# Optimization experiments

Measured on AMD Instinct MI355X. Metric: run time of the kernel, lower is better.

## Reference

```python
import jax, jax.numpy as jnp
import numpy as np

B = 4
N_PER_B = 65536
N = B * N_PER_B
GROUP_SIZE = 64
ORDER = 9  # min bits to cover grid size 512
C0, C1, C2 = 64, 128, 128


def hilbert_encode(coors, order):
    """Skilling AxesToTranspose, vectorized over N points, 3 dims -> int32 code."""
    n = 3
    X = [coors[:, i].astype(jnp.int32) for i in range(n)]
    M = 1 << (order - 1)
    Q = M
    while Q > 1:
        P = Q - 1
        for i in range(n):
            cond = (X[i] & Q) != 0
            if i == 0:
                X[0] = jnp.where(cond, X[0] ^ P, X[0])
            else:
                t = (X[0] ^ X[i]) & P
                x0 = jnp.where(cond, X[0] ^ P, X[0] ^ t)
                xi = jnp.where(cond, X[i], X[i] ^ t)
                X[0], X[i] = x0, xi
        Q >>= 1
    for i in range(1, n):
        X[i] = X[i] ^ X[i - 1]
    t = jnp.zeros_like(X[0])
    Q = M
    while Q > 1:
        t = jnp.where((X[n - 1] & Q) != 0, t ^ (Q - 1), t)
        Q >>= 1
    X = [x ^ t for x in X]
    # interleave transposed bits MSB-first: code has 3*order bits (27 < 31, fits int32)
    code = jnp.zeros_like(X[0])
    for b in range(order - 1, -1, -1):
        for i in range(n):
            code = (code << 1) | ((X[i] >> b) & 1)
    return code


def _mapping_indices(vox_coors):
    """Two Hilbert orderings (normal + reversed coord axes); per-batch stable grouping."""
    batch = vox_coors[:, 0]
    c1 = vox_coors[:, 1:4]
    c2 = vox_coors[:, 3:0:-1]  # [0,3,2,1] reverse of the xyz columns
    code1 = hilbert_encode(c1, ORDER)
    code2 = hilbert_encode(c2, ORDER)
    ind1 = jnp.lexsort((code1, batch))  # batch-major, curve-order minor
    ind2 = jnp.lexsort((code2, batch))
    inv1 = jnp.argsort(ind1)
    ind12 = inv1[ind2]  # maps ordering-1 arrangement to ordering-2 arrangement
    return ind1, ind12


def _block(p, x, params):
    """VoxFormer-style block: center pts per group, pos-encode, gate feats, local attn, FFN."""
    Wpos, bpos, Wq, Wk, Wv, Wo, Wout = params
    C = Wq.shape[0]
    gs = GROUP_SIZE
    pg = p.reshape(-1, gs, 3)
    e = (pg - pg.mean(axis=1, keepdims=True)).reshape(-1, 3) @ Wpos + bpos  # [N,C]
    h = (x * e).reshape(-1, gs, C)  # [G,gs,C]
    q, k, v = h @ Wq, h @ Wk, h @ Wv
    scores = jnp.einsum('gqc,gkc->gqk', q, k) / jnp.sqrt(jnp.asarray(C, q.dtype))
    attn = jax.nn.softmax(scores, axis=-1)
    o = jnp.einsum('gqk,gkc->gqc', attn, v).reshape(-1, C) @ Wo
    return jax.nn.relu(o) @ Wout  # [N,C_out]


def setup_inputs() -> dict:
    key = jax.random.key(0)
    ks = jax.random.split(key, 20)
    bcol = jnp.repeat(jnp.arange(B, dtype=jnp.int32), N_PER_B)
    z = jax.random.randint(ks[0], (N,), 0, 64, dtype=jnp.int32)
    y = jax.random.randint(ks[1], (N,), 0, 512, dtype=jnp.int32)
    x = jax.random.randint(ks[2], (N,), 0, 512, dtype=jnp.int32)
    vox_coors = jnp.stack([bcol, z, y, x], axis=1)
    vox_numbs = jnp.full((B,), N_PER_B, dtype=jnp.int32)
    vox_feats = jax.random.normal(ks[3], (N, C0), dtype=jnp.float32)
    pts_coors = jax.random.normal(ks[4], (N, 3), dtype=jnp.float32)
    s = lambda k, shape: jax.random.normal(k, shape, dtype=jnp.float32) / np.float32(np.sqrt(shape[0]))
    return dict(
        vox_numbs=vox_numbs, vox_coors=vox_coors, vox_feats=vox_feats, pts_coors=pts_coors,
        Wpos1=s(ks[5], (3, C0)), bpos1=jnp.zeros((C0,), jnp.float32),
        Wq1=s(ks[6], (C0, C0)), Wk1=s(ks[7], (C0, C0)), Wv1=s(ks[8], (C0, C0)),
        Wo1=s(ks[9], (C0, C0)), Wout1=s(ks[10], (C0, C1)),
        Wpos2=s(ks[11], (3, C1)), bpos2=jnp.zeros((C1,), jnp.float32),
        Wq2=s(ks[12], (C1, C1)), Wk2=s(ks[13], (C1, C1)), Wv2=s(ks[14], (C1, C1)),
        Wo2=s(ks[15], (C1, C1)), Wout2=s(ks[16], (C1, C2)),
    )


def reference(vox_numbs, vox_coors, vox_feats, pts_coors,
              Wpos1, bpos1, Wq1, Wk1, Wv1, Wo1, Wout1,
              Wpos2, bpos2, Wq2, Wk2, Wv2, Wo2, Wout2):
    ind1, ind12 = _mapping_indices(vox_coors)
    params = ((Wpos1, bpos1, Wq1, Wk1, Wv1, Wo1, Wout1),
              (Wpos2, bpos2, Wq2, Wk2, Wv2, Wo2, Wout2))
    for ind, prm in zip((ind1, ind12), params):
        vox_feats = vox_feats[ind]
        pts_coors = pts_coors[ind]
        vox_coors = vox_coors[ind]
        vox_feats = _block(pts_coors, vox_feats, prm)
    return vox_feats, pts_coors, vox_coors, vox_numbs
```

## Files before the change

### kernel.cpp

```cpp
#include <hip/hip_runtime.h>

using u64 = unsigned long long;
typedef _Float16 f16;
using f16x8 = __attribute__((ext_vector_type(8))) _Float16;
using f16x4 = __attribute__((ext_vector_type(4))) _Float16;
using f32x4 = __attribute__((ext_vector_type(4))) float;

__device__ __forceinline__ int hilbert3(int X0, int X1, int X2) {
  #pragma unroll
  for (int Q = 256; Q > 1; Q >>= 1) {
    const int P = Q - 1;
    if (X0 & Q) X0 ^= P;
    int t1 = (X0 ^ X1) & P;
    if (X1 & Q) X0 ^= P; else { X0 ^= t1; X1 ^= t1; }
    int t2 = (X0 ^ X2) & P;
    if (X2 & Q) X0 ^= P; else { X0 ^= t2; X2 ^= t2; }
  }
  X1 ^= X0;
  X2 ^= X1;
  int t = 0;
  #pragma unroll
  for (int Q = 256; Q > 1; Q >>= 1) if (X2 & Q) t ^= (Q - 1);
  X0 ^= t; X1 ^= t; X2 ^= t;
  int code = 0;
  #pragma unroll
  for (int b = 8; b >= 0; b--)
    code = (code << 3) | (((X0 >> b) & 1) << 2) | (((X1 >> b) & 1) << 1) | ((X2 >> b) & 1);
  return code;
}

__device__ __forceinline__ void cswap(u64& a, u64& b, bool up) {
  if ((a > b) == up) { u64 t = a; a = b; b = t; }
}

__global__ __launch_bounds__(1024) void sort_tile0(const int* __restrict__ vox,
                                                   u64* __restrict__ keys, int n,
                                                   int spanm1) {
  __shared__ u64 s[4096];
  const int base = blockIdx.x * 4096;
  const int bl = base & spanm1;
  #pragma unroll
  for (int m = 0; m < 4; m++) {
    const int e = base + threadIdx.x + m * 1024;
    const int isrc = e & (n - 1);
    const int4 c = ((const int4*)vox)[isrc];
    const unsigned code = (e < n) ? (unsigned)hilbert3(c.y, c.z, c.w)
                                  : (unsigned)hilbert3(c.w, c.z, c.y);
    s[threadIdx.x + m * 1024] =
        ((u64)(unsigned)c.x << 45) | ((u64)code << 18) | (unsigned)isrc;
  }
  __syncthreads();
  for (int k = 2; k <= 4096; k <<= 1) {
    for (int j = k >> 1; j >= 1; j >>= 1) {
      #pragma unroll
      for (int m = 0; m < 2; m++) {
        const int p = threadIdx.x + m * 1024;
        const int i = ((p & ~(j - 1)) << 1) | (p & (j - 1));
        const bool up = (((bl + i) & k) == 0);
        u64 a = s[i], b = s[i | j];
        if ((a > b) == up) { s[i] = b; s[i | j] = a; }
      }
      __syncthreads();
    }
  }
  #pragma unroll
  for (int m = 0; m < 4; m++)
    keys[base + threadIdx.x + m * 1024] = s[threadIdx.x + m * 1024];
}

template<int LEV>
__device__ __forceinline__ void gstepT(u64* __restrict__ keys, int t, int jlow,
                                       int k, int spanm1) {
  constexpr int S = 1 << LEV;
  const int i0 = ((t & ~(jlow - 1)) << LEV) | (t & (jlow - 1));
  const bool up = (((i0 & spanm1) & k) == 0);
  u64 x[S];
  #pragma unroll
  for (int m = 0; m < S; m++) x[m] = keys[i0 + (size_t)m * jlow];
  #pragma unroll
  for (int d = S >> 1; d >= 1; d >>= 1)
    #pragma unroll
    for (int m = 0; m < S; m++)
      if (!(m & d)) cswap(x[m], x[m | d], up);
  #pragma unroll
  for (int m = 0; m < S; m++) keys[i0 + (size_t)m * jlow] = x[m];
}

__global__ void bitonic_gN(u64* __restrict__ keys, int jlow, int lev, int k, int spanm1) {
  const int t = blockIdx.x * blockDim.x + threadIdx.x;
  switch (lev) {
    case 1: gstepT<1>(keys, t, jlow, k, spanm1); break;
    case 2: gstepT<2>(keys, t, jlow, k, spanm1); break;
    case 3: gstepT<3>(keys, t, jlow, k, spanm1); break;
    default: gstepT<4>(keys, t, jlow, k, spanm1); break;
  }
}

__global__ __launch_bounds__(1024) void merge_tile4(u64* __restrict__ keys, int k,
                                                    int spanm1) {
  __shared__ u64 s[4096];
  const int base = blockIdx.x * 4096;
  #pragma unroll
  for (int m = 0; m < 4; m++)
    s[threadIdx.x + m * 1024] = keys[base + threadIdx.x + m * 1024];
  __syncthreads();
  const bool up = (((base & spanm1) & k) == 0);
  for (int j = 2048; j >= 1; j >>= 1) {
    #pragma unroll
    for (int m = 0; m < 2; m++) {
      const int p = threadIdx.x + m * 1024;
      const int i = ((p & ~(j - 1)) << 1) | (p & (j - 1));
      u64 a = s[i], b = s[i | j];
      if ((a > b) == up) { s[i] = b; s[i | j] = a; }
    }
    __syncthreads();
  }
  #pragma unroll
  for (int m = 0; m < 4; m++)
    keys[base + threadIdx.x + m * 1024] = s[threadIdx.x + m * 1024];
}

__global__ void extract_inv_k(const u64* __restrict__ keys, const float* __restrict__ pts,
                              int* __restrict__ ind, int* __restrict__ inv,
                              float* __restrict__ pts1p, int n) {
  int t = blockIdx.x * blockDim.x + threadIdx.x;
  if (t >= n) return;
  int s = (int)(keys[t] & 0x3FFFFULL);
  ind[t] = s;
  inv[s] = t;
  pts1p[t * 3 + 0] = pts[s * 3 + 0];
  pts1p[t * 3 + 1] = pts[s * 3 + 1];
  pts1p[t * 3 + 2] = pts[s * 3 + 2];
}

__global__ void finish_k(const u64* __restrict__ keys2, const int* __restrict__ inv1,
                         int* __restrict__ g2, const float* __restrict__ pts,
                         const int* __restrict__ vox, const int* __restrict__ numbs,
                         float* __restrict__ out_pts, float* __restrict__ out_vox,
                         float* __restrict__ out_nb, int n, int B) {
  int t = blockIdx.x * blockDim.x + threadIdx.x;
  if (t >= n) return;
  int s = (int)(keys2[t] & 0x3FFFFULL);
  g2[t] = inv1[s];
  out_pts[t * 3 + 0] = pts[s * 3 + 0];
  out_pts[t * 3 + 1] = pts[s * 3 + 1];
  out_pts[t * 3 + 2] = pts[s * 3 + 2];
  const int4 v = ((const int4*)vox)[s];
  out_vox[t * 4 + 0] = (float)v.x;
  out_vox[t * 4 + 1] = (float)v.y;
  out_vox[t * 4 + 2] = (float)v.z;
  out_vox[t * 4 + 3] = (float)v.w;
  if (t < B) out_nb[t] = (float)numbs[t];
}

__global__ void prep_all(const float* __restrict__ Wq1, const float* __restrict__ Wk1,
                         const float* __restrict__ Wv1, const float* __restrict__ Wo1,
                         const float* __restrict__ Wout1,
                         const float* __restrict__ Wq2, const float* __restrict__ Wk2,
                         const float* __restrict__ Wv2, const float* __restrict__ Wo2,
                         const float* __restrict__ Wout2,
                         f16* __restrict__ A1a, f16* __restrict__ A2a, f16* __restrict__ A3a,
                         f16* __restrict__ A1b, f16* __restrict__ A2b, f16* __restrict__ A3b) {
  const int idx = blockIdx.x * blockDim.x + threadIdx.x;
  if (idx < 4096) {
    const int a = idx >> 6, b = idx & 63;
    float s1 = 0.f, s2 = 0.f;
    for (int c = 0; c < 64; c++) {
      s1 = fmaf(Wq1[b * 64 + c], Wk1[a * 64 + c], s1);
      s2 = fmaf(Wv1[b * 64 + c], Wo1[c * 64 + a], s2);
    }
    A1a[idx] = (f16)(s1 * 0.125f);
    A2a[idx] = (f16)s2;
  }
  if (idx < 8192) {
    const int o = idx >> 6, c = idx & 63;
    A3a[idx] = (f16)Wout1[c * 128 + o];
  }
  {
    const int a = idx >> 7, b = idx & 127;
    float s1 = 0.f, s2 = 0.f;
    for (int c = 0; c < 128; c++) {
      s1 = fmaf(Wq2[b * 128 + c], Wk2[a * 128 + c], s1);
      s2 = fmaf(Wv2[b * 128 + c], Wo2[c * 128 + a], s2);
    }
    A1b[idx] = (f16)(s1 * 0.08838834764831845f);
    A2b[idx] = (f16)s2;
    A3b[idx] = (f16)Wout2[b * 128 + a];
  }
}

__device__ __forceinline__ int swzb(int row) {
  return (((row & 7) ^ (((row >> 3) & 3) << 1)) << 4);
}

template<int M, int K, int AMODE>
__device__ __forceinline__ void gemmT(const f16* __restrict__ lA,
                                      const f16* __restrict__ lB, int w, int lane,
                                      f32x4 (&acc)[M / 64][4]) {
  constexpr int CT = M / 64;
  const int lr = lane & 15, lk = lane >> 4;
  #pragma unroll
  for (int ks = 0; ks < K / 32; ks++) {
    const int k0 = ks * 32 + lk * 8;
    f16x8 Af[CT];
    #pragma unroll
    for (int ct = 0; ct < CT; ct++) {
      const int c = lr + (w * CT + ct) * 16;
      if (AMODE == 1) {
        Af[ct] = *(const f16x8*)((const char*)lA + (((c * K + k0) * 2) ^ swzb(c)));
      } else {
        f16x8 a;
        #pragma unroll
        for (int e = 0; e < 8; e++) {
          const int j = k0 + e;
          a[e] = *(const f16*)((const char*)lA + (((j * M + c) * 2) ^ swzb(j)));
        }
        Af[ct] = a;
      }
    }
    f16x8 Bf[4];
    #pragma unroll
    for (int qt = 0; qt < 4; qt++) {
      const int q = lr + qt * 16;
      Bf[qt] = *(const f16x8*)((const char*)lB + (((q * K + k0) * 2) ^ swzb(q)));
    }
    __builtin_amdgcn_s_setprio(1);
    #pragma unroll
    for (int ct = 0; ct < CT; ct++)
      #pragma unroll
      for (int qt = 0; qt < 4; qt++)
        acc[ct][qt] = __builtin_amdgcn_mfma_f32_16x16x32_f16(Af[ct], Bf[qt], acc[ct][qt], 0, 0, 0);
    __builtin_amdgcn_s_setprio(0);
  }
}

template<int M, int K>
__device__ __forceinline__ void gemmPre(const f16x8 (&Af)[K / 32][M / 64],
                                        const f16* __restrict__ lB, int lane,
                                        f32x4 (&acc)[M / 64][4]) {
  constexpr int CT = M / 64;
  const int lr = lane & 15, lk = lane >> 4;
  #pragma unroll
  for (int ks = 0; ks < K / 32; ks++) {
    const int k0 = ks * 32 + lk * 8;
    f16x8 Bf[4];
    #pragma unroll
    for (int qt = 0; qt < 4; qt++) {
      const int q = lr + qt * 16;
      Bf[qt] = *(const f16x8*)((const char*)lB + (((q * K + k0) * 2) ^ swzb(q)));
    }
    __builtin_amdgcn_s_setprio(1);
    #pragma unroll
    for (int ct = 0; ct < CT; ct++)
      #pragma unroll
      for (int qt = 0; qt < 4; qt++)
        acc[ct][qt] = __builtin_amdgcn_mfma_f32_16x16x32_f16(Af[ks][ct], Bf[qt], acc[ct][qt], 0, 0, 0);
    __builtin_amdgcn_s_setprio(0);
  }
}

template<int M, int K>
__device__ __forceinline__ void loadA(const f16* __restrict__ Ag, int w, int lane,
                                      f16x8 (&Af)[K / 32][M / 64]) {
  constexpr int CT = M / 64;
  const int lr = lane & 15, lk = lane >> 4;
  #pragma unroll
  for (int ks = 0; ks < K / 32; ks++)
    #pragma unroll
    for (int ct = 0; ct < CT; ct++)
      Af[ks][ct] = *(const f16x8*)(Ag + (size_t)(lr + (w * CT + ct) * 16) * K + ks * 32 + lk * 8);
}

template<int M, bool RELU>
__device__ __forceinline__ void storeT16(f16* __restrict__ dst, int w, int lane,
                                         const f32x4 (&acc)[M / 64][4]) {
  constexpr int CT = M / 64;
  #pragma unroll
  for (int ct = 0; ct < CT; ct++)
    #pragma unroll
    for (int qt = 0; qt < 4; qt++) {
      const int q = (lane & 15) + qt * 16;
      const int c0 = (w * CT + ct) * 16 + (lane >> 4) * 4;
      f16x4 v;
      #pragma unroll
      for (int r = 0; r < 4; r++) {
        float x = acc[ct][qt][r];
        if (RELU) x = fmaxf(x, 0.f);
        v[r] = (f16)x;
      }
      *(f16x4*)((char*)dst + (((q * M + c0) * 2) ^ swzb(q))) = v;
    }
}

template<int C, bool X16, bool OUT16>
__global__ __launch_bounds__(512, 4) void block_mfma(
    const int* __restrict__ idx_x, const float* __restrict__ ptsP,
    const void* __restrict__ xsrc,
    const float* __restrict__ Wpos, const float* __restrict__ bpos,
    const f16* __restrict__ A1, const f16* __restrict__ A2, const f16* __restrict__ A3,
    void* __restrict__ outp) {
  constexpr int CT = C / 64;
  constexpr int GSZ = 64 * C * 4 + 8192;
  extern __shared__ char smem_raw[];
  char* smem = smem_raw + (threadIdx.x >> 8) * GSZ;
  f16* bufH = (f16*)smem;
  f16* bufT = bufH + 64 * C;
  f16* scH  = bufT + 64 * C;

  const int g = blockIdx.x * 2 + (threadIdx.x >> 8);
  const int t = threadIdx.x & 255;
  const int lane = t & 63;
  const int w = t >> 6;

  f16x8 A1f[C / 32][CT], A2f[C / 32][CT];
  loadA<C, C>(A1, w, lane, A1f);
  loadA<C, C>(A2, w, lane, A2f);

  const int q = t >> 2, qq = t & 3;
  const int sx = idx_x[g * 64 + q];
  f16x8 xr16[C / 32];
  float xv32[X16 ? 1 : C / 4];
  if (X16) {
    #pragma unroll
    for (int i = 0; i < C / 32; i++)
      xr16[i] = *(const f16x8*)((const f16*)xsrc + (size_t)sx * C + qq * (C / 4) + i * 8);
  } else {
    #pragma unroll
    for (int i = 0; i < C / 16; i++) {
      float4 x0 = *(const float4*)((const float*)xsrc + (size_t)sx * C + qq * (C / 4) + i * 4);
      xv32[i * 4 + 0] = x0.x; xv32[i * 4 + 1] = x0.y;
      xv32[i * 4 + 2] = x0.z; xv32[i * 4 + 3] = x0.w;
    }
  }

  {
    float mx = ptsP[(g * 64 + lane) * 3 + 0];
    float my = ptsP[(g * 64 + lane) * 3 + 1];
    float mz = ptsP[(g * 64 + lane) * 3 + 2];
    #pragma unroll
    for (int o = 32; o > 0; o >>= 1) {
      mx += __shfl_xor(mx, o); my += __shfl_xor(my, o); mz += __shfl_xor(mz, o);
    }
    mx *= (1.f / 64.f); my *= (1.f / 64.f); mz *= (1.f / 64.f);

    const float d0 = ptsP[(g * 64 + q) * 3 + 0] - mx;
    const float d1 = ptsP[(g * 64 + q) * 3 + 1] - my;
    const float d2 = ptsP[(g * 64 + q) * 3 + 2] - mz;
    #pragma unroll
    for (int i = 0; i < C / 32; i++) {
      const int c0 = qq * (C / 4) + i * 8;
      f16x8 hv;
      #pragma unroll
      for (int jj = 0; jj < 8; jj += 4) {
        const float4 w0 = *(const float4*)(Wpos + 0 * C + c0 + jj);
        const float4 w1 = *(const float4*)(Wpos + 1 * C + c0 + jj);
        const float4 w2 = *(const float4*)(Wpos + 2 * C + c0 + jj);
        const float4 bb = *(const float4*)(bpos + c0 + jj);
        float xa = X16 ? (float)xr16[i][jj + 0] : xv32[i * 8 + jj + 0];
        float xb = X16 ? (float)xr16[i][jj + 1] : xv32[i * 8 + jj + 1];
        float xc = X16 ? (float)xr16[i][jj + 2] : xv32[i * 8 + jj + 2];
        float xd = X16 ? (float)xr16[i][jj + 3] : xv32[i * 8 + jj + 3];
        hv[jj + 0] = (f16)(xa * fmaf(d0, w0.x, fmaf(d1, w1.x, fmaf(d2, w2.x, bb.x))));
        hv[jj + 1] = (f16)(xb * fmaf(d0, w0.y, fmaf(d1, w1.y, fmaf(d2, w2.y, bb.y))));
        hv[jj + 2] = (f16)(xc * fmaf(d0, w0.z, fmaf(d1, w1.z, fmaf(d2, w2.z, bb.z))));
        hv[jj + 3] = (f16)(xd * fmaf(d0, w0.w, fmaf(d1, w1.w, fmaf(d2, w2.w, bb.w))));
      }
      *(f16x8*)((char*)bufH + (((q * C + c0) * 2) ^ swzb(q))) = hv;
    }
  }
  __syncthreads();

  {
    f32x4 acc[CT][4] = {};
    gemmPre<C, C>(A1f, bufH, lane, acc);
    storeT16<C, false>(bufT, w, lane, acc);
  }
  __syncthreads();

  {
    f32x4 acc[1][4] = {};
    gemmT<64, C, 1>(bufH, bufT, w, lane, acc);
    const int lr = lane & 15, lk = lane >> 4;
    #pragma unroll
    for (int qt = 0; qt < 4; qt++) {
      const int qr = lr + qt * 16;
      const int j0 = w * 16 + lk * 4;
      f16x4 v;
      #pragma unroll
      for (int r = 0; r < 4; r++) v[r] = (f16)acc[0][qt][r];
      *(f16x4*)((char*)scH + (((qr * 64 + j0) * 2) ^ swzb(qr))) = v;
    }
  }
  __syncthreads();

  {
    float v[16];
    float mxv = -3.0e38f;
    #pragma unroll
    for (int i = 0; i < 2; i++) {
      f16x8 x8 = *(const f16x8*)((const char*)scH + (((q * 64 + qq * 16 + i * 8) * 2) ^ swzb(q)));
      #pragma unroll
      for (int j = 0; j < 8; j++) {
        v[i * 8 + j] = (float)x8[j];
        mxv = fmaxf(mxv, v[i * 8 + j]);
      }
    }
    mxv = fmaxf(mxv, __shfl_xor(mxv, 1));
    mxv = fmaxf(mxv, __shfl_xor(mxv, 2));
    float s = 0.f;
    #pragma unroll
    for (int i = 0; i < 16; i++) { v[i] = __expf(v[i] - mxv); s += v[i]; }
    s += __shfl_xor(s, 1);
    s += __shfl_xor(s, 2);
    const float inv = 1.f / s;
    #pragma unroll
    for (int i = 0; i < 2; i++) {
      f16x8 pk;
      #pragma unroll
      for (int j = 0; j < 8; j++) pk[j] = (f16)(v[i * 8 + j] * inv);
      *(f16x8*)((char*)scH + (((q * 64 + qq * 16 + i * 8) * 2) ^ swzb(q))) = pk;
    }
  }
  __syncthreads();

  {
    f32x4 acc[CT][4] = {};
    gemmT<C, 64, 2>(bufH, scH, w, lane, acc);
    storeT16<C, false>(bufT, w, lane, acc);
  }

  f16x8 A3f[C / 32][2];
  loadA<128, C>(A3, w, lane, A3f);
  __syncthreads();

  {
    f32x4 acc[CT][4] = {};
    gemmPre<C, C>(A2f, bufT, lane, acc);
    storeT16<C, true>(bufH, w, lane, acc);
  }
  __syncthreads();

  {
    f32x4 acc[2][4] = {};
    gemmPre<128, C>(A3f, bufH, lane, acc);
    #pragma unroll
    for (int ct = 0; ct < 2; ct++)
      #pragma unroll
      for (int qt = 0; qt < 4; qt++) {
        const int qr = (lane & 15) + qt * 16;
        const int o0 = (w * 2 + ct) * 16 + (lane >> 4) * 4;
        const size_t row = (size_t)g * 64 + qr;
        if (OUT16) {
          f16x4 v;
          #pragma unroll
          for (int r = 0; r < 4; r++) v[r] = (f16)acc[ct][qt][r];
          *(f16x4*)((f16*)outp + row * 128 + o0) = v;
        } else {
          *(f32x4*)((float*)outp + row * 128 + o0) = acc[ct][qt];
        }
      }
  }
}

extern "C" void kernel_launch(void* const* d_in, const int* in_sizes, int n_in,
                              void* d_out, int out_size, void* d_ws, size_t ws_size,
                              hipStream_t stream) {
  const int*   vox_numbs = (const int*)d_in[0];
  const int*   vox_coors = (const int*)d_in[1];
  const float* vox_feats = (const float*)d_in[2];
  const float* pts_coors = (const float*)d_in[3];
  const float* Wpos1 = (const float*)d_in[4];
  const float* bpos1 = (const float*)d_in[5];
  const float* Wq1   = (const float*)d_in[6];
  const float* Wk1   = (const float*)d_in[7];
  const float* Wv1   = (const float*)d_in[8];
  const float* Wo1   = (const float*)d_in[9];
  const float* Wout1 = (const float*)d_in[10];
  const float* Wpos2 = (const float*)d_in[11];
  const float* bpos2 = (const float*)d_in[12];
  const float* Wq2   = (const float*)d_in[13];
  const float* Wk2   = (const float*)d_in[14];
  const float* Wv2   = (const float*)d_in[15];
  const float* Wo2   = (const float*)d_in[16];
  const float* Wout2 = (const float*)d_in[17];

  const int B = in_sizes[0];
  const int n = in_sizes[1] / 4;
  const int ngrp = n / 64;

  char* w = (char*)d_ws;
  auto alloc = [&](size_t bytes) {
    char* p = w;
    w += (bytes + 255) & ~(size_t)255;
    return p;
  };
  u64* keys    = (u64*)alloc((size_t)2 * n * 8);
  int* ind1    = (int*)alloc((size_t)n * 4);
  int* inv1    = (int*)alloc((size_t)n * 4);
  int* g2      = (int*)alloc((size_t)n * 4);
  float* pts1p = (float*)alloc((size_t)n * 3 * 4);
  f16* A1a     = (f16*)alloc(64 * 64 * 2);
  f16* A2a     = (f16*)alloc(64 * 64 * 2);
  f16* A3a     = (f16*)alloc(128 * 64 * 2);
  f16* A1b     = (f16*)alloc(128 * 128 * 2);
  f16* A2b     = (f16*)alloc(128 * 128 * 2);
  f16* A3b     = (f16*)alloc(128 * 128 * 2);
  f16* feats1  = (f16*)alloc((size_t)n * 128 * 2);
  u64* keys2   = keys + n;

  float* out_feats = (float*)d_out;
  float* out_pts   = out_feats + (size_t)n * 128;
  float* out_vox   = out_pts + (size_t)n * 3;
  float* out_nb    = out_vox + (size_t)n * 4;

  auto f64k  = block_mfma<64,  false, true>;
  auto f128k = block_mfma<128, true,  false>;
  hipFuncSetAttribute((const void*)f64k,  hipFuncAttributeMaxDynamicSharedMemorySize, 65536);
  hipFuncSetAttribute((const void*)f128k, hipFuncAttributeMaxDynamicSharedMemorySize, 98304);

  prep_all<<<64, 256, 0, stream>>>(Wq1, Wk1, Wv1, Wo1, Wout1, Wq2, Wk2, Wv2, Wo2, Wout2,
                                   A1a, A2a, A3a, A1b, A2b, A3b);

  int span = (B > 0) ? n / B : n;
  if (span < 8192 || (span & (span - 1)) != 0 || n % span != 0) span = n;
  const int spanm1 = span - 1;

  sort_tile0<<<2 * n / 4096, 1024, 0, stream>>>(vox_coors, keys, n, spanm1);
  for (int k = 8192; k <= span; k <<= 1) {
    int j = k >> 1;
    while (j >= 4096) {
      int lev = 1;
      while (lev < 4 && (j >> lev) >= 4096) lev++;
      const int jlow = j >> (lev - 1);
      const int nth = (2 * n) >> lev;
      bitonic_gN<<<nth / 256, 256, 0, stream>>>(keys, jlow, lev, k, spanm1);
      j = jlow >> 1;
    }
    merge_tile4<<<2 * n / 4096, 1024, 0, stream>>>(keys, k, spanm1);
  }

  extract_inv_k<<<(n + 255) / 256, 256, 0, stream>>>(keys, pts_coors, ind1, inv1, pts1p, n);
  finish_k<<<(n + 255) / 256, 256, 0, stream>>>(keys2, inv1, g2, pts_coors, vox_coors,
                                                vox_numbs, out_pts, out_vox, out_nb, n, B);

  block_mfma<64, false, true><<<ngrp / 2, 512, 2 * 24576, stream>>>(
      ind1, pts1p, vox_feats, Wpos1, bpos1, A1a, A2a, A3a, feats1);
  block_mfma<128, true, false><<<ngrp / 2, 512, 2 * 40960, stream>>>(
      g2, out_pts, feats1, Wpos2, bpos2, A1b, A2b, A3b, out_feats);
}
```

Measured before the change: 322.8 us.

## Make block kernels persistent with prefetch of next group's inputs

Each block kernel now runs one 64-point group per 256-thread block and loops persistently over groups, with the grid capped at 1024 blocks. The previous launch packed two groups into 512 threads. While the first GEMM of the current group runs, the loop prefetches the next group's gathered features, point coordinates and centroid into registers and shared memory, hiding gather latency. A2/A3 weight fragments are loaded lazily inside the loop to cut register pressure, and launch bounds are adjusted per channel width. The risks are fewer resident groups per CU, an extra barrier per iteration, and reloading the weight fragments for every group.

Measured after the change: 671.6 us. 108% more time.

```diff
diff --git a/kernel.cpp b/kernel.cpp
--- a/kernel.cpp
+++ b/kernel.cpp
@@ -292,47 +292,49 @@
     }
 }
 
-template<int C, bool X16, bool OUT16>
-__global__ __launch_bounds__(512, 4) void block_mfma(
+template<int C, bool X16, bool OUT16, int MINW>
+__global__ __launch_bounds__(256, MINW) void block_mfma(
     const int* __restrict__ idx_x, const float* __restrict__ ptsP,
     const void* __restrict__ xsrc,
     const float* __restrict__ Wpos, const float* __restrict__ bpos,
     const f16* __restrict__ A1, const f16* __restrict__ A2, const f16* __restrict__ A3,
-    void* __restrict__ outp) {
+    void* __restrict__ outp, int ngrp, int nblk) {
   constexpr int CT = C / 64;
-  constexpr int GSZ = 64 * C * 4 + 8192;
-  extern __shared__ char smem_raw[];
-  char* smem = smem_raw + (threadIdx.x >> 8) * GSZ;
+  extern __shared__ char smem[];
   f16* bufH = (f16*)smem;
   f16* bufT = bufH + 64 * C;
   f16* scH  = bufT + 64 * C;
-
-  const int g = blockIdx.x * 2 + (threadIdx.x >> 8);
-  const int t = threadIdx.x & 255;
+  float* meanB = (float*)(scH + 64 * 64);
+
+  const int t = threadIdx.x;
   const int lane = t & 63;
   const int w = t >> 6;
-
-  f16x8 A1f[C / 32][CT], A2f[C / 32][CT];
+  const int q = t >> 2, qq = t & 3;
+
+  f16x8 A1f[C / 32][CT];
   loadA<C, C>(A1, w, lane, A1f);
-  loadA<C, C>(A2, w, lane, A2f);
-
-  const int q = t >> 2, qq = t & 3;
-  const int sx = idx_x[g * 64 + q];
-  f16x8 xr16[C / 32];
-  float xv32[X16 ? 1 : C / 4];
-  if (X16) {
+
+  int g = blockIdx.x;
+  if (g >= ngrp) return;
+
+  int sx = idx_x[g * 64 + q];
+  f16x8 xr[X16 ? C / 32 : 1];
+  float xv[X16 ? 1 : C / 4];
+  if constexpr (X16) {
     #pragma unroll
     for (int i = 0; i < C / 32; i++)
-      xr16[i] = *(const f16x8*)((const f16*)xsrc + (size_t)sx * C + qq * (C / 4) + i * 8);
+      xr[i] = *(const f16x8*)((const f16*)xsrc + (size_t)sx * C + qq * (C / 4) + i * 8);
   } else {
     #pragma unroll
     for (int i = 0; i < C / 16; i++) {
       float4 x0 = *(const float4*)((const float*)xsrc + (size_t)sx * C + qq * (C / 4) + i * 4);
-      xv32[i * 4 + 0] = x0.x; xv32[i * 4 + 1] = x0.y;
-      xv32[i * 4 + 2] = x0.z; xv32[i * 4 + 3] = x0.w;
-    }
-  }
-
+      xv[i * 4 + 0] = x0.x; xv[i * 4 + 1] = x0.y;
+      xv[i * 4 + 2] = x0.z; xv[i * 4 + 3] = x0.w;
+    }
+  }
+  float pq0 = ptsP[(g * 64 + q) * 3 + 0];
+  float pq1 = ptsP[(g * 64 + q) * 3 + 1];
+  float pq2 = ptsP[(g * 64 + q) * 3 + 2];
   {
     float mx = ptsP[(g * 64 + lane) * 3 + 0];
     float my = ptsP[(g * 64 + lane) * 3 + 1];
@@ -341,124 +343,189 @@
     for (int o = 32; o > 0; o >>= 1) {
       mx += __shfl_xor(mx, o); my += __shfl_xor(my, o); mz += __shfl_xor(mz, o);
     }
-    mx *= (1.f / 64.f); my *= (1.f / 64.f); mz *= (1.f / 64.f);
-
-    const float d0 = ptsP[(g * 64 + q) * 3 + 0] - mx;
-    const float d1 = ptsP[(g * 64 + q) * 3 + 1] - my;
-    const float d2 = ptsP[(g * 64 + q) * 3 + 2] - mz;
-    #pragma unroll
-    for (int i = 0; i < C / 32; i++) {
-      const int c0 = qq * (C / 4) + i * 8;
-      f16x8 hv;
-      #pragma unroll
-      for (int jj = 0; jj < 8; jj += 4) {
-        const float4 w0 = *(const float4*)(Wpos + 0 * C + c0 + jj);
-        const float4 w1 = *(const float4*)(Wpos + 1 * C + c0 + jj);
-        const float4 w2 = *(const float4*)(Wpos + 2 * C + c0 + jj);
-        const float4 bb = *(const float4*)(bpos + c0 + jj);
-        float xa = X16 ? (float)xr16[i][jj + 0] : xv32[i * 8 + jj + 0];
-        float xb = X16 ? (float)xr16[i][jj + 1] : xv32[i * 8 + jj + 1];
-        float xc = X16 ? (float)xr16[i][jj + 2] : xv32[i * 8 + jj + 2];
-        float xd = X16 ? (float)xr16[i][jj + 3] : xv32[i * 8 + jj + 3];
-        hv[jj + 0] = (f16)(xa * fmaf(d0, w0.x, fmaf(d1, w1.x, fmaf(d2, w2.x, bb.x))));
-        hv[jj + 1] = (f16)(xb * fmaf(d0, w0.y, fmaf(d1, w1.y, fmaf(d2, w2.y, bb.y))));
-        hv[jj + 2] = (f16)(xc * fmaf(d0, w0.z, fmaf(d1, w1.z, fmaf(d2, w2.z, bb.z))));
-        hv[jj + 3] = (f16)(xd * fmaf(d0, w0.w, fmaf(d1, w1.w, fmaf(d2, w2.w, bb.w))));
-      }
-      *(f16x8*)((char*)bufH + (((q * C + c0) * 2) ^ swzb(q))) = hv;
+    if (t == 0) {
+      meanB[0] = mx * (1.f / 64.f);
+      meanB[1] = my * (1.f / 64.f);
+      meanB[2] = mz * (1.f / 64.f);
     }
   }
   __syncthreads();
 
-  {
-    f32x4 acc[CT][4] = {};
-    gemmPre<C, C>(A1f, bufH, lane, acc);
-    storeT16<C, false>(bufT, w, lane, acc);
-  }
-  __syncthreads();
-
-  {
-    f32x4 acc[1][4] = {};
-    gemmT<64, C, 1>(bufH, bufT, w, lane, acc);
-    const int lr = lane & 15, lk = lane >> 4;
-    #pragma unroll
-    for (int qt = 0; qt < 4; qt++) {
-      const int qr = lr + qt * 16;
-      const int j0 = w * 16 + lk * 4;
-      f16x4 v;
-      #pragma unroll
-      for (int r = 0; r < 4; r++) v[r] = (f16)acc[0][qt][r];
-      *(f16x4*)((char*)scH + (((qr * 64 + j0) * 2) ^ swzb(qr))) = v;
-    }
-  }
-  __syncthreads();
-
-  {
-    float v[16];
-    float mxv = -3.0e38f;
-    #pragma unroll
-    for (int i = 0; i < 2; i++) {
-      f16x8 x8 = *(const f16x8*)((const char*)scH + (((q * 64 + qq * 16 + i * 8) * 2) ^ swzb(q)));
-      #pragma unroll
-      for (int j = 0; j < 8; j++) {
-        v[i * 8 + j] = (float)x8[j];
-        mxv = fmaxf(mxv, v[i * 8 + j]);
-      }
-    }
-    mxv = fmaxf(mxv, __shfl_xor(mxv, 1));
-    mxv = fmaxf(mxv, __shfl_xor(mxv, 2));
-    float s = 0.f;
-    #pragma unroll
-    for (int i = 0; i < 16; i++) { v[i] = __expf(v[i] - mxv); s += v[i]; }
-    s += __shfl_xor(s, 1);
-    s += __shfl_xor(s, 2);
-    const float inv = 1.f / s;
-    #pragma unroll
-    for (int i = 0; i < 2; i++) {
-      f16x8 pk;
-      #pragma unroll
-      for (int j = 0; j < 8; j++) pk[j] = (f16)(v[i * 8 + j] * inv);
-      *(f16x8*)((char*)scH + (((q * 64 + qq * 16 + i * 8) * 2) ^ swzb(q))) = pk;
-    }
-  }
-  __syncthreads();
-
-  {
-    f32x4 acc[CT][4] = {};
-    gemmT<C, 64, 2>(bufH, scH, w, lane, acc);
-    storeT16<C, false>(bufT, w, lane, acc);
-  }
-
-  f16x8 A3f[C / 32][2];
-  loadA<128, C>(A3, w, lane, A3f);
-  __syncthreads();
-
-  {
-    f32x4 acc[CT][4] = {};
-    gemmPre<C, C>(A2f, bufT, lane, acc);
-    storeT16<C, true>(bufH, w, lane, acc);
-  }
-  __syncthreads();
-
-  {
-    f32x4 acc[2][4] = {};
-    gemmPre<128, C>(A3f, bufH, lane, acc);
-    #pragma unroll
-    for (int ct = 0; ct < 2; ct++)
+  while (true) {
+    const int gn = g + nblk;
+    const bool more = gn < ngrp;
+
+    {
+      const float d0 = pq0 - meanB[0];
+      const float d1 = pq1 - meanB[1];
+      const float d2 = pq2 - meanB[2];
+      #pragma unroll
+      for (int i = 0; i < C / 32; i++) {
+        const int c0 = qq * (C / 4) + i * 8;
+        f16x8 hv;
+        #pragma unroll
+        for (int jj = 0; jj < 8; jj += 4) {
+          const float4 w0 = *(const float4*)(Wpos + 0 * C + c0 + jj);
+          const float4 w1 = *(const float4*)(Wpos + 1 * C + c0 + jj);
+          const float4 w2 = *(const float4*)(Wpos + 2 * C + c0 + jj);
+          const float4 bb = *(const float4*)(bpos + c0 + jj);
+          float xa, xb, xc, xd;
+          if constexpr (X16) {
+            xa = (float)xr[i][jj + 0]; xb = (float)xr[i][jj + 1];
+            xc = (float)xr[i][jj + 2]; xd = (float)xr[i][jj + 3];
+          } else {
+            xa = xv[i * 8 + jj + 0]; xb = xv[i * 8 + jj + 1];
+            xc = xv[i * 8 + jj + 2]; xd = xv[i * 8 + jj + 3];
+          }
+          hv[jj + 0] = (f16)(xa * fmaf(d0, w0.x, fmaf(d1, w1.x, fmaf(d2, w2.x, bb.x))));
+          hv[jj + 1] = (f16)(xb * fmaf(d0, w0.y, fmaf(d1, w1.y, fmaf(d2, w2.y, bb.y))));
+          hv[jj + 2] = (f16)(xc * fmaf(d0, w0.z, fmaf(d1, w1.z, fmaf(d2, w2.z, bb.z))));
+          hv[jj + 3] = (f16)(xd * fmaf(d0, w0.w, fmaf(d1, w1.w, fmaf(d2, w2.w, bb.w))));
+        }
+        *(f16x8*)((char*)bufH + (((q * C + c0) * 2) ^ swzb(q))) = hv;
+      }
+    }
+    int sxN = 0;
+    if (more) sxN = idx_x[gn * 64 + q];
+    __syncthreads();
+
+    {
+      f32x4 acc[CT][4] = {};
+      gemmPre<C, C>(A1f, bufH, lane, acc);
+      storeT16<C, false>(bufT, w, lane, acc);
+    }
+
+    f16x8 xrN[X16 ? C / 32 : 1];
+    float xvN[X16 ? 1 : C / 4];
+    float pqN0 = 0.f, pqN1 = 0.f, pqN2 = 0.f;
+    if (more) {
+      if constexpr (X16) {
+        #pragma unroll
+        for (int i = 0; i < C / 32; i++)
+          xrN[i] = *(const f16x8*)((const f16*)xsrc + (size_t)sxN * C + qq * (C / 4) + i * 8);
+      } else {
+        #pragma unroll
+        for (int i = 0; i < C / 16; i++) {
+          float4 x0 = *(const float4*)((const float*)xsrc + (size_t)sxN * C + qq * (C / 4) + i * 4);
+          xvN[i * 4 + 0] = x0.x; xvN[i * 4 + 1] = x0.y;
+          xvN[i * 4 + 2] = x0.z; xvN[i * 4 + 3] = x0.w;
+        }
+      }
+      pqN0 = ptsP[(gn * 64 + q) * 3 + 0];
+      pqN1 = ptsP[(gn * 64 + q) * 3 + 1];
+      pqN2 = ptsP[(gn * 64 + q) * 3 + 2];
+      float mx = ptsP[(gn * 64 + lane) * 3 + 0];
+      float my = ptsP[(gn * 64 + lane) * 3 + 1];
+      float mz = ptsP[(gn * 64 + lane) * 3 + 2];
+      #pragma unroll
+      for (int o = 32; o > 0; o >>= 1) {
+        mx += __shfl_xor(mx, o); my += __shfl_xor(my, o); mz += __shfl_xor(mz, o);
+      }
+      if (t == 0) {
+        meanB[0] = mx * (1.f / 64.f);
+        meanB[1] = my * (1.f / 64.f);
+        meanB[2] = mz * (1.f / 64.f);
+      }
+    }
+    __syncthreads();
+
+    {
+      f32x4 acc[1][4] = {};
+      gemmT<64, C, 1>(bufH, bufT, w, lane, acc);
+      const int lr = lane & 15, lk = lane >> 4;
       #pragma unroll
       for (int qt = 0; qt < 4; qt++) {
-        const int qr = (lane & 15) + qt * 16;
-        const int o0 = (w * 2 + ct) * 16 + (lane >> 4) * 4;
-        const size_t row = (size_t)g * 64 + qr;
-        if (OUT16) {
-          f16x4 v;
-          #pragma unroll
-          for (int r = 0; r < 4; r++) v[r] = (f16)acc[ct][qt][r];
-          *(f16x4*)((f16*)outp + row * 128 + o0) = v;
-        } else {
-          *(f32x4*)((float*)outp + row * 128 + o0) = acc[ct][qt];
+        const int qr = lr + qt * 16;
+        const int j0 = w * 16 + lk * 4;
+        f16x4 v;
+        #pragma unroll
+        for (int r = 0; r < 4; r++) v[r] = (f16)acc[0][qt][r];
+        *(f16x4*)((char*)scH + (((qr * 64 + j0) * 2) ^ swzb(qr))) = v;
+      }
+    }
+    __syncthreads();
+
+    {
+      float v[16];
+      float mxv = -3.0e38f;
+      #pragma unroll
+      for (int i = 0; i < 2; i++) {
+        f16x8 x8 = *(const f16x8*)((const char*)scH + (((q * 64 + qq * 16 + i * 8) * 2) ^ swzb(q)));
+        #pragma unroll
+        for (int j = 0; j < 8; j++) {
+          v[i * 8 + j] = (float)x8[j];
+          mxv = fmaxf(mxv, v[i * 8 + j]);
         }
       }
+      mxv = fmaxf(mxv, __shfl_xor(mxv, 1));
+      mxv = fmaxf(mxv, __shfl_xor(mxv, 2));
+      float s = 0.f;
+      #pragma unroll
+      for (int i = 0; i < 16; i++) { v[i] = __expf(v[i] - mxv); s += v[i]; }
+      s += __shfl_xor(s, 1);
+      s += __shfl_xor(s, 2);
+      const float inv = 1.f / s;
+      #pragma unroll
+      for (int i = 0; i < 2; i++) {
+        f16x8 pk;
+        #pragma unroll
+        for (int j = 0; j < 8; j++) pk[j] = (f16)(v[i * 8 + j] * inv);
+        *(f16x8*)((char*)scH + (((q * 64 + qq * 16 + i * 8) * 2) ^ swzb(q))) = pk;
+      }
+    }
+    __syncthreads();
+
+    f16x8 A2f[C / 32][CT];
+    loadA<C, C>(A2, w, lane, A2f);
+
+    {
+      f32x4 acc[CT][4] = {};
+      gemmT<C, 64, 2>(bufH, scH, w, lane, acc);
+      storeT16<C, false>(bufT, w, lane, acc);
+    }
+    __syncthreads();
+
+    {
+      f32x4 acc[CT][4] = {};
+      gemmPre<C, C>(A2f, bufT, lane, acc);
+      storeT16<C, true>(bufH, w, lane, acc);
+    }
+    f16x8 A3f[C / 32][2];
+    loadA<128, C>(A3, w, lane, A3f);
+    __syncthreads();
+
+    {
+      f32x4 acc[2][4] = {};
+      gemmPre<128, C>(A3f, bufH, lane, acc);
+      #pragma unroll
+      for (int ct = 0; ct < 2; ct++)
+        #pragma unroll
+        for (int qt = 0; qt < 4; qt++) {
+          const int qr = (lane & 15) + qt * 16;
+          const int o0 = (w * 2 + ct) * 16 + (lane >> 4) * 4;
+          const size_t row = (size_t)g * 64 + qr;
+          if (OUT16) {
+            f16x4 v;
+            #pragma unroll
+            for (int r = 0; r < 4; r++) v[r] = (f16)acc[ct][qt][r];
+            *(f16x4*)((f16*)outp + row * 128 + o0) = v;
+          } else {
+            *(f32x4*)((float*)outp + row * 128 + o0) = acc[ct][qt];
+          }
+        }
+    }
+
+    if (!more) break;
+    __syncthreads();
+    g = gn;
+    if constexpr (X16) {
+      #pragma unroll
+      for (int i = 0; i < C / 32; i++) xr[i] = xrN[i];
+    } else {
+      #pragma unroll
+      for (int i = 0; i < C / 4; i++) xv[i] = xvN[i];
+    }
+    pq0 = pqN0; pq1 = pqN1; pq2 = pqN2;
   }
 }
 
@@ -513,10 +580,10 @@
   float* out_vox   = out_pts + (size_t)n * 3;
   float* out_nb    = out_vox + (size_t)n * 4;
 
-  auto f64k  = block_mfma<64,  false, true>;
-  auto f128k = block_mfma<128, true,  false>;
-  hipFuncSetAttribute((const void*)f64k,  hipFuncAttributeMaxDynamicSharedMemorySize, 65536);
-  hipFuncSetAttribute((const void*)f128k, hipFuncAttributeMaxDynamicSharedMemorySize, 98304);
+  auto f64k  = block_mfma<64,  false, true,  4>;
+  auto f128k = block_mfma<128, true,  false, 3>;
+  hipFuncSetAttribute((const void*)f64k,  hipFuncAttributeMaxDynamicSharedMemorySize, 32768);
+  hipFuncSetAttribute((const void*)f128k, hipFuncAttributeMaxDynamicSharedMemorySize, 49152);
 
   prep_all<<<64, 256, 0, stream>>>(Wq1, Wk1, Wv1, Wo1, Wout1, Wq2, Wk2, Wv2, Wo2, Wout2,
                                    A1a, A2a, A3a, A1b, A2b, A3b);
@@ -543,8 +610,9 @@
   finish_k<<<(n + 255) / 256, 256, 0, stream>>>(keys2, inv1, g2, pts_coors, vox_coors,
                                                 vox_numbs, out_pts, out_vox, out_nb, n, B);
 
-  block_mfma<64, false, true><<<ngrp / 2, 512, 2 * 24576, stream>>>(
-      ind1, pts1p, vox_feats, Wpos1, bpos1, A1a, A2a, A3a, feats1);
-  block_mfma<128, true, false><<<ngrp / 2, 512, 2 * 40960, stream>>>(
-      g2, out_pts, feats1, Wpos2, bpos2, A1b, A2b, A3b, out_feats);
-}
+  const int nblk = (ngrp < 1024) ? ngrp : 1024;
+  block_mfma<64, false, true, 4><<<nblk, 256, 24592, stream>>>(
+      ind1, pts1p, vox_feats, Wpos1, bpos1, A1a, A2a, A3a, feats1, ngrp, nblk);
+  block_mfma<128, true, false, 3><<<nblk, 256, 40976, stream>>>(
+      g2, out_pts, feats1, Wpos2, bpos2, A1b, A2b, A3b, out_feats, ngrp, nblk);
+}
```
